# Optimization experiments

Hardware: AMD Instinct MI355X
Metric: run time of the kernel (lower is better)

Reference implementation:

```python
import jax, jax.numpy as jnp
import numpy as np

NUM_HEADS = 8
HIDDEN = 8

def conv1x1(x, w):
    # x: [B,C,H,W], w: [O,C] -> [B,O,H,W]
    return jnp.einsum('oc,bchw->bohw', w, x)

def grid_sample_border(img, gx, gy):
    # Bilinear grid_sample, padding_mode='border', align_corners=True.
    # img: [B,C,H,W]; gx, gy: [B,H,W] normalized coords in [-1,1].
    B, C, H, W = img.shape
    ix = (gx + 1.0) * 0.5 * (W - 1)
    iy = (gy + 1.0) * 0.5 * (H - 1)
    x0f = jnp.floor(ix); y0f = jnp.floor(iy)
    wx = (ix - x0f)[..., None]; wy = (iy - y0f)[..., None]
    x0 = x0f.astype(jnp.int32); y0 = y0f.astype(jnp.int32)
    x0c = jnp.clip(x0, 0, W - 1); x1c = jnp.clip(x0 + 1, 0, W - 1)
    y0c = jnp.clip(y0, 0, H - 1); y1c = jnp.clip(y0 + 1, 0, H - 1)
    imt = jnp.transpose(img, (0, 2, 3, 1))  # [B,H,W,C]
    b = jnp.arange(B)[:, None, None]
    v00 = imt[b, y0c, x0c]; v01 = imt[b, y0c, x1c]
    v10 = imt[b, y1c, x0c]; v11 = imt[b, y1c, x1c]
    out = (v00 * (1 - wx) * (1 - wy) + v01 * wx * (1 - wy)
           + v10 * (1 - wx) * wy + v11 * wx * wy)
    return jnp.transpose(out, (0, 3, 1, 2))

def process_sub(cur, ref, Wq, Wk, Wv, Wver, Whor):
    B, C, H, W = cur.shape
    c = HIDDEN // NUM_HEADS  # per-head channel dim (=1)
    q = conv1x1(cur, Wq).reshape(B, NUM_HEADS, c, H, W)
    k = conv1x1(ref, Wk).reshape(B, NUM_HEADS, c, H, W)
    v = conv1x1(ref, Wv).reshape(B, NUM_HEADS, c, H, W)
    # vertical axial attention (each column w independent, attend over rows)
    a_ver = jax.nn.softmax(jnp.einsum('bkchw,bkclw->bkwhl', q, k), axis=-1)
    o_ver = jnp.einsum('bkwhl,bkclw->bkchw', a_ver, v).reshape(B, HIDDEN, H, W)
    o_ver = conv1x1(o_ver, Wver)[:, 0]  # [B,H,W]
    # horizontal axial attention (each row h independent, attend over cols)
    a_hor = jax.nn.softmax(jnp.einsum('bkchw,bkchl->bkhwl', q, k), axis=-1)
    o_hor = jnp.einsum('bkhwl,bkchl->bkchw', a_hor, v).reshape(B, HIDDEN, H, W)
    o_hor = conv1x1(o_hor, Whor)[:, 0]  # [B,H,W]
    # identity grid + flow
    ys = -1.0 + 2.0 * jnp.arange(H, dtype=cur.dtype) / max(float(H - 1), 1.0)
    xs = -1.0 + 2.0 * jnp.arange(W, dtype=cur.dtype) / max(float(W - 1), 1.0)
    gx = xs[None, None, :] + o_hor / ((W - 1.0) / 2.0)
    gy = ys[None, :, None] + o_ver / ((H - 1.0) / 2.0)
    return grid_sample_border(ref, gx, gy)

def _forward(cur_fea, ref_fea, Wq, Wk, Wv, Wver, Whor):
    B, C, H, W = cur_fea.shape
    def split(x):
        return jnp.stack([x[:, :, ::2, ::2], x[:, :, 1::2, 1::2],
                          x[:, :, ::2, 1::2], x[:, :, 1::2, ::2]], 0)
    cur_sub = split(cur_fea).reshape(4 * B, C, H // 2, W // 2)
    ref_sub = split(ref_fea).reshape(4 * B, C, H // 2, W // 2)
    warped = process_sub(cur_sub, ref_sub, Wq, Wk, Wv, Wver, Whor)
    ul, br, ur, bl = warped.reshape(4, B, C, H // 2, W // 2)
    out = jnp.zeros((B, C, H, W), dtype=jnp.float32)
    out = out.at[:, :, ::2, ::2].set(ul)
    out = out.at[:, :, ::2, 1::2].set(ur)
    out = out.at[:, :, 1::2, ::2].set(bl)
    out = out.at[:, :, 1::2, 1::2].set(br)
    return out

def setup_inputs() -> dict:
    key = jax.random.key(0)
    ks = jax.random.split(key, 7)
    B, C, H, W = 2, 64, 256, 256
    return {
        'cur_fea': jax.random.normal(ks[0], (B, C, H, W), jnp.float32),
        'ref_fea': jax.random.normal(ks[1], (B, C, H, W), jnp.float32),
        'Wq': jax.random.normal(ks[2], (HIDDEN, C), jnp.float32) * 0.05,
        'Wk': jax.random.normal(ks[3], (HIDDEN, C), jnp.float32) * 0.05,
        'Wv': jax.random.normal(ks[4], (HIDDEN, C), jnp.float32) * 0.05,
        'Wver': jax.random.normal(ks[5], (1, HIDDEN), jnp.float32) * 0.05,
        'Whor': jax.random.normal(ks[6], (1, HIDDEN), jnp.float32) * 0.05,
    }

def reference(cur_fea, ref_fea, Wq, Wk, Wv, Wver, Whor):
    return _forward(cur_fea, ref_fea, Wq, Wk, Wv, Wver, Whor)
```

## Files before the change

### kernel.cpp

```cpp
#include <hip/hip_runtime.h>


constexpr int PLANE = 16384;
constexpr float LOG2E = 1.4426950408889634f;

typedef float v2f __attribute__((ext_vector_type(2)));

static __device__ __forceinline__ v2f pk_mul(v2f a, v2f b) {
    v2f d;
    asm("v_pk_mul_f32 %0, %1, %2" : "=v"(d) : "v"(a), "v"(b));
    return d;
}
static __device__ __forceinline__ v2f pk_add(v2f a, v2f b) {
    v2f d;
    asm("v_pk_add_f32 %0, %1, %2" : "=v"(d) : "v"(a), "v"(b));
    return d;
}
static __device__ __forceinline__ v2f pk_fma(v2f a, v2f b, v2f c) {
    v2f d;
    asm("v_pk_fma_f32 %0, %1, %2, %3" : "=v"(d) : "v"(a), "v"(b), "v"(c));
    return d;
}

__global__ __launch_bounds__(512) void qkv_kernel(
    const float* __restrict__ cur, const float* __restrict__ ref,
    const float* __restrict__ Wq, const float* __restrict__ Wk,
    const float* __restrict__ Wv,
    float* __restrict__ Q, float* __restrict__ K, float* __restrict__ V)
{
    __shared__ float WT[64 * 24];
    __shared__ float red0[128 * 25];
    __shared__ float red1[128 * 25];
    const int tid = threadIdx.x;
    for (int i = tid; i < 64 * 24; i += 512) {
        int c = i / 24, j = i % 24;
        float val = (j < 8) ? Wq[j * 64 + c]
                  : (j < 16) ? LOG2E * Wk[(j - 8) * 64 + c]
                  : Wv[(j - 16) * 64 + c];
        WT[c * 24 + j] = val;
    }
    __syncthreads();

    const int bi = blockIdx.x;
    const int b  = bi >> 9;
    const int Y  = (bi >> 1) & 255;
    const int Xh = bi & 1;
    const int cg = tid >> 7;
    const int xi = tid & 127;
    const int X  = Xh * 128 + xi;

    const size_t base_in = (size_t)b * 64 * 65536 + (size_t)Y * 256 + X;
    const float* curp = cur + base_in;
    const float* refp = ref + base_in;

    float q[8], k[8], v[8];
#pragma unroll
    for (int i = 0; i < 8; ++i) { q[i] = 0.f; k[i] = 0.f; v[i] = 0.f; }

    const int c0 = cg * 16;
#pragma unroll 8
    for (int c = 0; c < 16; ++c) {
        float cu = curp[(size_t)(c0 + c) * 65536];
        float rf = refp[(size_t)(c0 + c) * 65536];
        const float* wr = &WT[(c0 + c) * 24];
#pragma unroll
        for (int i = 0; i < 8; ++i) {
            q[i] = fmaf(wr[i],      cu, q[i]);
            k[i] = fmaf(wr[8 + i],  rf, k[i]);
            v[i] = fmaf(wr[16 + i], rf, v[i]);
        }
    }

    float* row0 = &red0[xi * 25];
    float* row1 = &red1[xi * 25];
    if (cg == 1) {
#pragma unroll
        for (int i = 0; i < 8; ++i) {
            row0[i] = q[i]; row0[8 + i] = k[i]; row0[16 + i] = v[i];
        }
    } else if (cg == 3) {
#pragma unroll
        for (int i = 0; i < 8; ++i) {
            row1[i] = q[i]; row1[8 + i] = k[i]; row1[16 + i] = v[i];
        }
    }
    __syncthreads();
    if (cg == 2) {
#pragma unroll
        for (int i = 0; i < 8; ++i) {
            row1[i]      += q[i];
            row1[8 + i]  += k[i];
            row1[16 + i] += v[i];
        }
    } else if (cg == 0) {
#pragma unroll
        for (int i = 0; i < 8; ++i) {
            q[i] += row0[i]; k[i] += row0[8 + i]; v[i] += row0[16 + i];
        }
    }
    __syncthreads();
    if (cg == 0) {
        const int dy = Y & 1, dx = X & 1;
        const int p  = dy ? (dx ? 1 : 3) : (dx ? 2 : 0);
        const int sb = p * 2 + b;
        const int h = Y >> 1, w = X >> 1;
#pragma unroll
        for (int i = 0; i < 8; ++i) {
            const size_t o = ((size_t)(sb * 8 + i) << 14) + (h << 7) + w;
            Q[o] = q[i] + row1[i];
            K[o] = k[i] + row1[8 + i];
            V[o] = v[i] + row1[16 + i];
        }
    }
}

__global__ __launch_bounds__(256) void transpose_kernel(
    const float* __restrict__ Q, const float* __restrict__ K,
    const float* __restrict__ V,
    float* __restrict__ QT, float* __restrict__ KT, float* __restrict__ VT)
{
    __shared__ float tile[32 * 33];
    const int bi = blockIdx.x;
    const int plane = bi >> 4;
    const int ti = (bi >> 2) & 3, tj = bi & 3;
    const int t = threadIdx.x;
    const int r = t >> 3, c4 = (t & 7) * 4;
    const size_t pb = (size_t)plane << 14;
    const size_t ibase = pb + (size_t)(ti * 32) * 128 + tj * 32;
    const size_t obase = pb + (size_t)(tj * 32) * 128 + ti * 32;

    const float* srcs[3] = { Q, K, V };
    float* dsts[3] = { QT, KT, VT };
#pragma unroll
    for (int a = 0; a < 3; ++a) {
        const float* src = srcs[a];
        float* dst = dsts[a];
        const float4 val = *(const float4*)&src[ibase + (size_t)r * 128 + c4];
        if (a) __syncthreads();
        tile[r * 33 + c4 + 0] = val.x;
        tile[r * 33 + c4 + 1] = val.y;
        tile[r * 33 + c4 + 2] = val.z;
        tile[r * 33 + c4 + 3] = val.w;
        __syncthreads();
        float4 o;
        o.x = tile[(c4 + 0) * 33 + r];
        o.y = tile[(c4 + 1) * 33 + r];
        o.z = tile[(c4 + 2) * 33 + r];
        o.w = tile[(c4 + 3) * 33 + r];
        *(float4*)&dst[obase + (size_t)r * 128 + c4] = o;
    }
}

__global__ __launch_bounds__(256) void attn_fused(
    const float* __restrict__ Q, const float* __restrict__ K,
    const float* __restrict__ V,
    const float* __restrict__ QT, const float* __restrict__ KT,
    const float* __restrict__ VT,
    const float* __restrict__ Whor, const float* __restrict__ Wver,
    float* __restrict__ OH, float* __restrict__ OVT)
{
    __shared__ __align__(16) float kk[8 * 128];
    __shared__ __align__(16) float vv[8 * 128];
    __shared__ float part[128];

    const int pass = blockIdx.x >> 10;
    const float* __restrict__ Qa = pass ? QT : Q;
    const float* __restrict__ Ka = pass ? KT : K;
    const float* __restrict__ Va = pass ? VT : V;
    const float* __restrict__ wsel = pass ? Wver : Whor;
    float* __restrict__ o = pass ? OVT : OH;

    const int tid  = threadIdx.x;
    const int sub  = tid >> 7;
    const int t    = tid & 127;
    const int sbl  = blockIdx.x & 1023;
    const int sb   = sbl >> 7;
    const int line = sbl & 127;

    const size_t base = (((size_t)(sb * 8)) << 14) + ((size_t)line << 7);
    {
        const int f  = tid;
        const int hh = f >> 5;
        const int tt = (f & 31) << 2;
        const size_t g = base + ((size_t)hh << 14) + tt;
        ((float4*)kk)[f] = *(const float4*)&Ka[g];
        ((float4*)vv)[f] = *(const float4*)&Va[g];
    }
    __syncthreads();

    float acc = 0.f;
#pragma unroll
    for (int i = 0; i < 4; ++i) {
        const int head = sub * 4 + i;
        const float s = Qa[base + ((size_t)head << 14) + t];
        const v2f sv = { s, s };
        const v2f* k2 = (const v2f*)&kk[head << 7];
        const v2f* v2 = (const v2f*)&vv[head << 7];
        v2f d01 = {0.f, 0.f}, d23 = {0.f, 0.f};
        v2f n01 = {0.f, 0.f}, n23 = {0.f, 0.f};
#pragma unroll 8
        for (int l = 0; l < 32; ++l) {
            const v2f k01 = k2[2 * l],     k23 = k2[2 * l + 1];
            const v2f vq01 = v2[2 * l],    vq23 = v2[2 * l + 1];
            const v2f a01 = pk_mul(sv, k01);
            const v2f a23 = pk_mul(sv, k23);
            const v2f e01 = { __builtin_amdgcn_exp2f(a01.x),
                              __builtin_amdgcn_exp2f(a01.y) };
            const v2f e23 = { __builtin_amdgcn_exp2f(a23.x),
                              __builtin_amdgcn_exp2f(a23.y) };
            d01 = pk_add(d01, e01);
            d23 = pk_add(d23, e23);
            n01 = pk_fma(e01, vq01, n01);
            n23 = pk_fma(e23, vq23, n23);
        }
        const v2f dv = pk_add(d01, d23), nv = pk_add(n01, n23);
        const float den = dv.x + dv.y;
        const float num = nv.x + nv.y;
        acc = fmaf(wsel[head], num * __builtin_amdgcn_rcpf(den), acc);
    }

    if (sub) part[t] = acc;
    __syncthreads();
    if (!sub) {
        o[((size_t)sb << 14) + ((size_t)line << 7) + t] = acc + part[t];
    }
}

__global__ __launch_bounds__(256) void warp_kernel(
    const float* __restrict__ ref, const float* __restrict__ ovt,
    const float* __restrict__ oh, float* __restrict__ out)
{
    const int bi = blockIdx.x;
    const int Y  = bi & 255;
    const int cg = (bi >> 8) & 3;
    const int b  = bi >> 10;
    const int X  = threadIdx.x;

    const int dy = Y & 1, dx = X & 1;
    const int p  = dy ? (dx ? 1 : 3) : (dx ? 2 : 0);
    const int sb = p * 2 + b;
    const int h = Y >> 1, w = X >> 1;

    const float ix = (float)w + oh [((size_t)sb << 14) + (h << 7) + w];
    const float iy = (float)h + ovt[((size_t)sb << 14) + (w << 7) + h];

    const float x0f = floorf(ix), y0f = floorf(iy);
    const float wx = ix - x0f,    wy = iy - y0f;
    const int x0 = (int)x0f, y0 = (int)y0f;
    const int x0c = min(max(x0, 0), 127),     x1c = min(max(x0 + 1, 0), 127);
    const int y0c = min(max(y0, 0), 127),     y1c = min(max(y0 + 1, 0), 127);

    const float w00 = (1.f - wx) * (1.f - wy);
    const float w01 = wx * (1.f - wy);
    const float w10 = (1.f - wx) * wy;
    const float w11 = wx * wy;

    const int cb  = min(2 * x0c, 252);
    const bool hi  = (x0c == 127);
    const bool up1 = hi | (x1c != x0c);
    const int r0 = (2 * y0c + dy) * 256, r1 = (2 * y1c + dy) * 256;
    const int dst = Y * 256 + X;

    const float* rp = ref + ((size_t)b * 64 + cg * 16) * 65536;
    float* op = out + ((size_t)b * 64 + cg * 16) * 65536;

#pragma unroll 4
    for (int c = 0; c < 16; ++c) {
        const size_t pl = (size_t)c * 65536;
        const float4 f0 = *(const float4*)&rp[pl + r0 + cb];
        const float4 f1 = *(const float4*)&rp[pl + r1 + cb];
        const float L0 = dx ? f0.y : f0.x, H0 = dx ? f0.w : f0.z;
        const float L1 = dx ? f1.y : f1.x, H1 = dx ? f1.w : f1.z;
        const float v00 = hi ? H0 : L0,  v01 = up1 ? H0 : L0;
        const float v10 = hi ? H1 : L1,  v11 = up1 ? H1 : L1;
        op[pl + dst] = fmaf(w00, v00, fmaf(w01, v01, fmaf(w10, v10, w11 * v11)));
    }
}

extern "C" void kernel_launch(void* const* d_in, const int* in_sizes, int n_in,
                              void* d_out, int out_size, void* d_ws, size_t ws_size,
                              hipStream_t stream)
{
    const float* cur  = (const float*)d_in[0];
    const float* ref  = (const float*)d_in[1];
    const float* Wq   = (const float*)d_in[2];
    const float* Wk   = (const float*)d_in[3];
    const float* Wv   = (const float*)d_in[4];
    const float* Wver = (const float*)d_in[5];
    const float* Whor = (const float*)d_in[6];
    float* out = (float*)d_out;

    float* ws = (float*)d_ws;
    const size_t NQ = 8 * 8 * (size_t)PLANE;
    float* Q   = ws;
    float* K   = Q  + NQ;
    float* V   = K  + NQ;
    float* QT  = V  + NQ;
    float* KT  = QT + NQ;
    float* VT  = KT + NQ;
    float* OVT = VT + NQ;
    float* OH  = OVT + 8 * (size_t)PLANE;

    qkv_kernel<<<1024, 512, 0, stream>>>(cur, ref, Wq, Wk, Wv, Q, K, V);
    transpose_kernel<<<1024, 256, 0, stream>>>(Q, K, V, QT, KT, VT);
    attn_fused<<<2048, 256, 0, stream>>>(Q, K, V, QT, KT, VT,
                                         Whor, Wver, OH, OVT);
    warp_kernel<<<2048, 256, 0, stream>>>(ref, OVT, OH, out);
}
```

Baseline: 188.7 us.

## Remove transpose kernel and read columns directly in vertical attention pass

Measured after the change: 179.2 us. 5.0% less time.

```diff
diff --git a/kernel.cpp b/kernel.cpp
--- a/kernel.cpp
+++ b/kernel.cpp
@@ -114,104 +114,83 @@
     }
 }
 
-__global__ __launch_bounds__(256) void transpose_kernel(
-    const float* __restrict__ Q, const float* __restrict__ K,
-    const float* __restrict__ V,
-    float* __restrict__ QT, float* __restrict__ KT, float* __restrict__ VT)
-{
-    __shared__ float tile[32 * 33];
-    const int bi = blockIdx.x;
-    const int plane = bi >> 4;
-    const int ti = (bi >> 2) & 3, tj = bi & 3;
-    const int t = threadIdx.x;
-    const int r = t >> 3, c4 = (t & 7) * 4;
-    const size_t pb = (size_t)plane << 14;
-    const size_t ibase = pb + (size_t)(ti * 32) * 128 + tj * 32;
-    const size_t obase = pb + (size_t)(tj * 32) * 128 + ti * 32;
-
-    const float* srcs[3] = { Q, K, V };
-    float* dsts[3] = { QT, KT, VT };
-#pragma unroll
-    for (int a = 0; a < 3; ++a) {
-        const float* src = srcs[a];
-        float* dst = dsts[a];
-        const float4 val = *(const float4*)&src[ibase + (size_t)r * 128 + c4];
-        if (a) __syncthreads();
-        tile[r * 33 + c4 + 0] = val.x;
-        tile[r * 33 + c4 + 1] = val.y;
-        tile[r * 33 + c4 + 2] = val.z;
-        tile[r * 33 + c4 + 3] = val.w;
-        __syncthreads();
-        float4 o;
-        o.x = tile[(c4 + 0) * 33 + r];
-        o.y = tile[(c4 + 1) * 33 + r];
-        o.z = tile[(c4 + 2) * 33 + r];
-        o.w = tile[(c4 + 3) * 33 + r];
-        *(float4*)&dst[obase + (size_t)r * 128 + c4] = o;
-    }
-}
-
 __global__ __launch_bounds__(256) void attn_fused(
     const float* __restrict__ Q, const float* __restrict__ K,
     const float* __restrict__ V,
-    const float* __restrict__ QT, const float* __restrict__ KT,
-    const float* __restrict__ VT,
     const float* __restrict__ Whor, const float* __restrict__ Wver,
     float* __restrict__ OH, float* __restrict__ OVT)
 {
-    __shared__ __align__(16) float kk[8 * 128];
-    __shared__ __align__(16) float vv[8 * 128];
+    __shared__ __align__(16) float kk[8 * 132];
+    __shared__ __align__(16) float vv[8 * 132];
     __shared__ float part[128];
 
     const int pass = blockIdx.x >> 10;
-    const float* __restrict__ Qa = pass ? QT : Q;
-    const float* __restrict__ Ka = pass ? KT : K;
-    const float* __restrict__ Va = pass ? VT : V;
+    const int P    = blockIdx.x & 1023;
+    int sb, line;
+    if (!pass) {
+        sb   = P >> 7;
+        line = P & 127;
+    } else {
+        const int w4 = P & 7, wl = P >> 6;
+        sb   = (P >> 3) & 7;
+        line = (w4 << 4) | wl;
+    }
     const float* __restrict__ wsel = pass ? Wver : Whor;
     float* __restrict__ o = pass ? OVT : OH;
 
-    const int tid  = threadIdx.x;
-    const int sub  = tid >> 7;
-    const int t    = tid & 127;
-    const int sbl  = blockIdx.x & 1023;
-    const int sb   = sbl >> 7;
-    const int line = sbl & 127;
-
-    const size_t base = (((size_t)(sb * 8)) << 14) + ((size_t)line << 7);
+    const int tid = threadIdx.x;
+    const int sub = tid >> 7;
+    const int t   = tid & 127;
+    const size_t sbb = ((size_t)(sb * 8)) << 14;
+
     {
-        const int f  = tid;
-        const int hh = f >> 5;
-        const int tt = (f & 31) << 2;
-        const size_t g = base + ((size_t)hh << 14) + tt;
-        ((float4*)kk)[f] = *(const float4*)&Ka[g];
-        ((float4*)vv)[f] = *(const float4*)&Va[g];
-    }
-    __syncthreads();
+        const int hh = tid >> 5;
+        const int fi = tid & 31;
+        if (!pass) {
+            const size_t g = sbb + ((size_t)hh << 14) + ((size_t)line << 7) + (fi << 2);
+            *(float4*)&kk[hh * 132 + (fi << 2)] = *(const float4*)&K[g];
+            *(float4*)&vv[hh * 132 + (fi << 2)] = *(const float4*)&V[g];
+        } else {
+            const size_t g = sbb + ((size_t)hh << 14) + ((size_t)(fi << 2) << 7) + line;
+            float4 kq, vq;
+            kq.x = K[g];       kq.y = K[g + 128];
+            kq.z = K[g + 256]; kq.w = K[g + 384];
+            vq.x = V[g];       vq.y = V[g + 128];
+            vq.z = V[g + 256]; vq.w = V[g + 384];
+            *(float4*)&kk[hh * 132 + (fi << 2)] = kq;
+            *(float4*)&vv[hh * 132 + (fi << 2)] = vq;
+        }
+    }
+    __syncthreads();
+
+    const float* __restrict__ sQ = pass
+        ? &Q[sbb + ((size_t)t << 7) + line]
+        : &Q[sbb + ((size_t)line << 7) + t];
 
     float acc = 0.f;
 #pragma unroll
     for (int i = 0; i < 4; ++i) {
         const int head = sub * 4 + i;
-        const float s = Qa[base + ((size_t)head << 14) + t];
+        const float s = sQ[(size_t)head << 14];
         const v2f sv = { s, s };
-        const v2f* k2 = (const v2f*)&kk[head << 7];
-        const v2f* v2 = (const v2f*)&vv[head << 7];
+        const float4* k4 = (const float4*)&kk[head * 132];
+        const float4* v4 = (const float4*)&vv[head * 132];
         v2f d01 = {0.f, 0.f}, d23 = {0.f, 0.f};
         v2f n01 = {0.f, 0.f}, n23 = {0.f, 0.f};
 #pragma unroll 8
         for (int l = 0; l < 32; ++l) {
-            const v2f k01 = k2[2 * l],     k23 = k2[2 * l + 1];
-            const v2f vq01 = v2[2 * l],    vq23 = v2[2 * l + 1];
-            const v2f a01 = pk_mul(sv, k01);
-            const v2f a23 = pk_mul(sv, k23);
+            const float4 kq = k4[l];
+            const float4 vq = v4[l];
+            const v2f a01 = pk_mul(sv, (v2f){kq.x, kq.y});
+            const v2f a23 = pk_mul(sv, (v2f){kq.z, kq.w});
             const v2f e01 = { __builtin_amdgcn_exp2f(a01.x),
                               __builtin_amdgcn_exp2f(a01.y) };
             const v2f e23 = { __builtin_amdgcn_exp2f(a23.x),
                               __builtin_amdgcn_exp2f(a23.y) };
             d01 = pk_add(d01, e01);
             d23 = pk_add(d23, e23);
-            n01 = pk_fma(e01, vq01, n01);
-            n23 = pk_fma(e23, vq23, n23);
+            n01 = pk_fma(e01, (v2f){vq.x, vq.y}, n01);
+            n23 = pk_fma(e23, (v2f){vq.z, vq.w}, n23);
         }
         const v2f dv = pk_add(d01, d23), nv = pk_add(n01, n23);
         const float den = dv.x + dv.y;
@@ -295,15 +274,10 @@
     float* Q   = ws;
     float* K   = Q  + NQ;
     float* V   = K  + NQ;
-    float* QT  = V  + NQ;
-    float* KT  = QT + NQ;
-    float* VT  = KT + NQ;
-    float* OVT = VT + NQ;
+    float* OVT = V  + NQ;
     float* OH  = OVT + 8 * (size_t)PLANE;
 
     qkv_kernel<<<1024, 512, 0, stream>>>(cur, ref, Wq, Wk, Wv, Q, K, V);
-    transpose_kernel<<<1024, 256, 0, stream>>>(Q, K, V, QT, KT, VT);
-    attn_fused<<<2048, 256, 0, stream>>>(Q, K, V, QT, KT, VT,
-                                         Whor, Wver, OH, OVT);
+    attn_fused<<<2048, 256, 0, stream>>>(Q, K, V, Whor, Wver, OH, OVT);
     warp_kernel<<<2048, 256, 0, stream>>>(ref, OVT, OH, out);
 }
```
